# Optimization experiments

Hardware: AMD Instinct MI355X
Metric: run time of the kernel (lower is better)

## Reference

```python
import jax, jax.numpy as jnp
import numpy as np

HIDDEN = 1024
HEADS = 16
HEAD_DIM = HIDDEN // HEADS
LN_EPS = 1e-12


def _layer_norm(x, gamma, beta, eps=LN_EPS):
    mu = jnp.mean(x, axis=-1, keepdims=True)
    var = jnp.var(x, axis=-1, keepdims=True)
    return (x - mu) * jax.lax.rsqrt(var + eps) * gamma + beta


def setup_inputs() -> dict:
    key = jax.random.key(0)
    ks = jax.random.split(key, 8)
    B, S = 4, 2048
    hidden_states = jax.random.normal(ks[0], (B, S, HIDDEN), dtype=jnp.float32)
    attention_mask = jnp.zeros((B, 1, 1, S), dtype=jnp.float32)
    scale = 1.0 / np.sqrt(HIDDEN)
    return {
        "hidden_states": hidden_states,
        "attention_mask": attention_mask,
        "ln_gamma": jnp.ones((HIDDEN,), jnp.float32),
        "ln_beta": jnp.zeros((HIDDEN,), jnp.float32),
        "W_qkv": jax.random.normal(ks[1], (HIDDEN, 3 * HIDDEN), jnp.float32) * scale,
        "b_qkv": jnp.zeros((3 * HIDDEN,), jnp.float32),
        "W_out": jax.random.normal(ks[2], (HIDDEN, HIDDEN), jnp.float32) * scale,
        "b_out": jnp.zeros((HIDDEN,), jnp.float32),
    }


def reference(hidden_states, attention_mask, ln_gamma, ln_beta, W_qkv, b_qkv, W_out, b_out):
    B, S, H = hidden_states.shape
    x = _layer_norm(hidden_states, ln_gamma, ln_beta)
    qkv = x @ W_qkv + b_qkv  # [B, S, 3H]
    q, k, v = jnp.split(qkv, 3, axis=-1)
    q = q.reshape(B, S, HEADS, HEAD_DIM)
    k = k.reshape(B, S, HEADS, HEAD_DIM)
    v = v.reshape(B, S, HEADS, HEAD_DIM)
    # scores: [B, heads, q_len, kv_len]
    scores = jnp.einsum("bqhd,bkhd->bhqk", q, k) * (1.0 / np.sqrt(HEAD_DIM))
    scores = scores + attention_mask
    probs = jax.nn.softmax(scores, axis=-1)
    attn = jnp.einsum("bhqk,bkhd->bqhd", probs, v).reshape(B, S, H)
    out = attn @ W_out + b_out
    out = out + hidden_states  # residual (dropout is identity at p=0)
    return out
```

## Files before the change

kernel.cpp:

```cpp
#include <hip/hip_runtime.h>

#define SEQ 2048
#define HID 1024
#define NHEAD 16
#define HDIM 64
#define NB 4
#define NTOK (NB * SEQ)
#define NQKV (3 * HID)
#define LOG2E 1.44269504088896f
#define QSCALE (0.125f * LOG2E)

typedef __attribute__((ext_vector_type(8))) short bf16x8;
typedef __attribute__((ext_vector_type(4))) float f32x4;


__device__ __forceinline__ void glds16(const void* g, void* l) {
  __builtin_amdgcn_global_load_lds(
      (const __attribute__((address_space(1))) void*)g,
      (__attribute__((address_space(3))) void*)l, 16, 0, 0);
}

__device__ __forceinline__ ushort f2bf(float f) {
  union { float f; unsigned int u; } a; a.f = f;
  unsigned int u = a.u;
  return (ushort)((u + 0x7fffu + ((u >> 16) & 1u)) >> 16);
}

__device__ __forceinline__ unsigned int pack2bf_rh(float a, float b) {
  return __builtin_amdgcn_perm(__float_as_uint(b) + 0x8000u,
                               __float_as_uint(a) + 0x8000u, 0x07060302u);
}


__global__ __launch_bounds__(256) void ln_kernel(const float* __restrict__ x,
                                                 const float* __restrict__ g,
                                                 const float* __restrict__ be,
                                                 ushort* __restrict__ y) {
  const int row = blockIdx.x;
  const int tid = threadIdx.x;
  const float4 v = ((const float4*)(x + (size_t)row * HID))[tid];
  float s  = v.x + v.y + v.z + v.w;
  float sq = v.x * v.x + v.y * v.y + v.z * v.z + v.w * v.w;
  for (int o = 1; o < 64; o <<= 1) { s += __shfl_xor(s, o, 64); sq += __shfl_xor(sq, o, 64); }
  __shared__ float as_[4], aq_[4];
  const int wv = tid >> 6;
  if ((tid & 63) == 0) { as_[wv] = s; aq_[wv] = sq; }
  __syncthreads();
  s  = as_[0] + as_[1] + as_[2] + as_[3];
  sq = aq_[0] + aq_[1] + aq_[2] + aq_[3];
  const float mu  = s * (1.0f / HID);
  const float var = sq * (1.0f / HID) - mu * mu;
  const float rs  = rsqrtf(var + 1e-12f);
  const float4 gv = ((const float4*)g)[tid];
  const float4 bv = ((const float4*)be)[tid];
  ushort4 o;
  o.x = f2bf((v.x - mu) * rs * gv.x + bv.x);
  o.y = f2bf((v.y - mu) * rs * gv.y + bv.y);
  o.z = f2bf((v.z - mu) * rs * gv.z + bv.z);
  o.w = f2bf((v.w - mu) * rs * gv.w + bv.w);
  ((ushort4*)(y + (size_t)row * HID))[tid] = o;
}


__global__ __launch_bounds__(256) void transpose_cvt2(const float* __restrict__ W0,
                                                      ushort* __restrict__ T0,
                                                      const float* __restrict__ W1,
                                                      ushort* __restrict__ T1) {
  const float* W; ushort* WT; int C;
  if (blockIdx.z == 0) { W = W0; WT = T0; C = NQKV; }
  else { if (blockIdx.x >= HID / 32) return; W = W1; WT = T1; C = HID; }
  const int R = HID;
  __shared__ float t[32][33];
  const int c0 = blockIdx.x * 32, r0 = blockIdx.y * 32;
  const int tx = threadIdx.x & 31, ty = threadIdx.x >> 5;
  for (int j = 0; j < 4; ++j)
    t[ty + j * 8][tx] = W[(size_t)(r0 + ty + j * 8) * C + c0 + tx];
  __syncthreads();
  for (int j = 0; j < 4; ++j)
    WT[(size_t)(c0 + ty + j * 8) * R + r0 + tx] = f2bf(t[tx][ty + j * 8]);
}


__global__ __launch_bounds__(256) void v_transpose(const ushort* __restrict__ qkv,
                                                   ushort* __restrict__ vt) {
  __shared__ ushort t[64][66];
  const int s0 = blockIdx.x * 64, h = blockIdx.y, b = blockIdx.z;
  const size_t tokbase = (size_t)b * SEQ;
  for (int e = 0; e < 2; ++e) {
    const int c = e * 256 + threadIdx.x;
    const int sr = c >> 3, dc = c & 7;
    *(uint4*)&t[sr][dc * 8] =
        *(const uint4*)(qkv + (tokbase + s0 + sr) * NQKV + 2 * HID + h * HDIM + dc * 8);
  }
  __syncthreads();
  for (int e = 0; e < 2; ++e) {
    const int c = e * 256 + threadIdx.x;
    const int dr = c >> 3, sc = c & 7;
    ushort tmp[8];
    for (int j = 0; j < 8; ++j) tmp[j] = t[sc * 8 + j][dr];
    *(uint4*)(vt + ((size_t)(b * NHEAD + h) * HDIM + dr) * SEQ + s0 + sc * 8) = *(uint4*)tmp;
  }
}


template <int MODE>
__global__ __launch_bounds__(256) void gemm_bt(const ushort* __restrict__ A,
                                               const ushort* __restrict__ Bt,
                                               const float* __restrict__ bias,
                                               const float* __restrict__ resid,
                                               ushort* __restrict__ obf,
                                               float* __restrict__ of32,
                                               int M, int N, int K) {
  __shared__ ushort As[128 * 64];
  __shared__ ushort Bs[128 * 64];
  const int tid = threadIdx.x;
  const int lane = tid & 63, wv = tid >> 6;
  const int q = lane >> 4, li = lane & 15;
  const int m0 = blockIdx.y * 128, n0 = blockIdx.x * 128;
  const int wm = (wv >> 1) * 64, wn = (wv & 1) * 64;
  f32x4 acc[4][4] = {};

  for (int kb = 0; kb < K; kb += 64) {
    for (int e = 0; e < 4; ++e) {
      const int chunk = (wv * 4 + e) * 64 + lane;
      const int row = chunk >> 3, slot = chunk & 7;
      const int kc = slot ^ (row & 7);
      glds16(A  + (size_t)(m0 + row) * K + kb + kc * 8, As + (wv * 4 + e) * 512);
      glds16(Bt + (size_t)(n0 + row) * K + kb + kc * 8, Bs + (wv * 4 + e) * 512);
    }
    __syncthreads();
    for (int ks = 0; ks < 2; ++ks) {
      const int kc = ks * 4 + q;
      bf16x8 af[4], bfr[4];
      for (int mi = 0; mi < 4; ++mi) {
        const int row = wm + mi * 16 + li;
        af[mi] = *(const bf16x8*)(As + (row * 8 + (kc ^ (row & 7))) * 8);
      }
      for (int ni = 0; ni < 4; ++ni) {
        const int row = wn + ni * 16 + li;
        bfr[ni] = *(const bf16x8*)(Bs + (row * 8 + (kc ^ (row & 7))) * 8);
      }
      for (int mi = 0; mi < 4; ++mi)
        for (int ni = 0; ni < 4; ++ni)
          acc[mi][ni] = __builtin_amdgcn_mfma_f32_16x16x32_bf16(af[mi], bfr[ni], acc[mi][ni], 0, 0, 0);
    }
    __syncthreads();
  }

  const float qs = (MODE == 0 && n0 < HID) ? QSCALE : 1.0f;
  for (int ni = 0; ni < 4; ++ni) {
    const int col = n0 + wn + ni * 16 + li;
    const float bvs = bias[col] * qs;
    for (int mi = 0; mi < 4; ++mi) {
      for (int r = 0; r < 4; ++r) {
        const int row = m0 + wm + mi * 16 + q * 4 + r;
        const float v = fmaf(acc[mi][ni][r], qs, bvs);
        if (MODE == 0) obf[(size_t)row * N + col] = f2bf(v);
        else           of32[(size_t)row * N + col] = v + resid[(size_t)row * N + col];
      }
    }
  }
}


__global__ __launch_bounds__(256) void flash_attn(const ushort* __restrict__ qkv,
                                                  const ushort* __restrict__ vt,
                                                  const float* __restrict__ mask,
                                                  ushort* __restrict__ outa) {
  __shared__ ushort KV[2][8192];
  const int tid = threadIdx.x, lane = tid & 63, wv = tid >> 6;
  const int quad = lane >> 4, li = lane & 15;
  const int wq = wv * 32;

  const int L = blockIdx.x + 16 * blockIdx.y + 256 * blockIdx.z;
  const int xcd = L & 7, rrem = L >> 3;
  const int p = (rrem >> 4) * 8 + xcd;
  const int qt = rrem & 15, h = p & 15, b = p >> 4;

  const size_t tokbase = (size_t)b * SEQ;
  const size_t vtbase = (size_t)(b * NHEAD + h) * HDIM * SEQ;
  const float* mrow = mask + (size_t)b * SEQ;

  for (int e = 0; e < 4; ++e) {
    const int c = (wv * 4 + e) * 64 + lane;
    const int row = c >> 3, slot = c & 7;
    const int kc = slot ^ (row & 7);
    glds16(qkv + (tokbase + qt * 128 + row) * NQKV + h * HDIM + kc * 8,
           &KV[0][0] + (wv * 4 + e) * 512);
  }
  __syncthreads();

  bf16x8 qf[2][2];
  for (int ks = 0; ks < 2; ++ks) {
    const int kc = ks * 4 + quad;
    for (int nq = 0; nq < 2; ++nq) {
      const int row = wq + nq * 16 + li;
      qf[ks][nq] = *(const bf16x8*)(&KV[0][0] + (row * 8 + (kc ^ (row & 7))) * 8);
    }
  }
  __syncthreads();

  int koff[2][4], voff[2][4];
  for (int ks = 0; ks < 2; ++ks) {
    const int kc = ks * 4 + quad;
    for (int i = 0; i < 4; ++i) {
      const int row = i * 16 + li;
      koff[ks][i] = (row * 8 + (kc ^ (row & 7))) * 8;
      voff[ks][i] = koff[ks][i] + 4096;
    }
  }
  const ushort* ksrc[2];
  const ushort* vsrc[2];
  for (int e = 0; e < 2; ++e) {
    const int c = (wv * 2 + e) * 64 + lane;
    const int row = c >> 3, slot = c & 7;
    const int kc = slot ^ (row & 7);
    const int gkv = (row & 0x23) | ((row & 0x0c) << 1) | ((row & 0x10) >> 2);
    ksrc[e] = qkv + (tokbase + gkv) * NQKV + HID + h * HDIM + kc * 8;
    vsrc[e] = vt + vtbase + (size_t)row * SEQ + kc * 8;
  }

  const unsigned int one2 = 0x3F803F80u;
  bf16x8 ones;
  for (int j = 0; j < 4; ++j) ((unsigned int*)&ones)[j] = one2;

  f32x4 accO[2][4] = {};
  f32x4 accL[2] = {};

  auto stage_kv = [&](int t, int buf) {
    const int kv0 = t * 64;
    for (int e = 0; e < 2; ++e) {
      glds16(ksrc[e] + (size_t)kv0 * NQKV, &KV[buf][0] + (wv * 2 + e) * 512);
      glds16(vsrc[e] + kv0,                &KV[buf][4096] + (wv * 2 + e) * 512);
    }
  };

  auto compute = [&](int t, int buf) {
    const int kv0 = t * 64;
    const ushort* Kb = &KV[buf][0];

    float4 mk[4];
    for (int mkv = 0; mkv < 4; ++mkv)
      mk[mkv] = *(const float4*)(mrow + kv0 + (mkv >> 1) * 32 + quad * 8 + (mkv & 1) * 4);

    f32x4 sc[2][4] = {};
    for (int ks = 0; ks < 2; ++ks) {
      bf16x8 kf[4];
      for (int mkv = 0; mkv < 4; ++mkv)
        kf[mkv] = *(const bf16x8*)(Kb + koff[ks][mkv]);
      for (int nq = 0; nq < 2; ++nq)
        for (int mkv = 0; mkv < 4; ++mkv)
          sc[nq][mkv] = __builtin_amdgcn_mfma_f32_16x16x32_bf16(kf[mkv], qf[ks][nq], sc[nq][mkv], 0, 0, 0);
    }

    unsigned int pk[2][4][2];
    for (int nq = 0; nq < 2; ++nq) {
      for (int mkv = 0; mkv < 4; ++mkv) {
        const float p0 = __builtin_amdgcn_exp2f(fmaf(mk[mkv].x, LOG2E, sc[nq][mkv][0]));
        const float p1 = __builtin_amdgcn_exp2f(fmaf(mk[mkv].y, LOG2E, sc[nq][mkv][1]));
        const float p2 = __builtin_amdgcn_exp2f(fmaf(mk[mkv].z, LOG2E, sc[nq][mkv][2]));
        const float p3 = __builtin_amdgcn_exp2f(fmaf(mk[mkv].w, LOG2E, sc[nq][mkv][3]));
        pk[nq][mkv][0] = pack2bf_rh(p0, p1);
        pk[nq][mkv][1] = pack2bf_rh(p2, p3);
      }
    }

    for (int ks = 0; ks < 2; ++ks) {
      bf16x8 vf[4];
      for (int nd = 0; nd < 4; ++nd)
        vf[nd] = *(const bf16x8*)(Kb + voff[ks][nd]);
      for (int mq = 0; mq < 2; ++mq) {
        bf16x8 pf;
        ((unsigned int*)&pf)[0] = pk[mq][2 * ks][0];
        ((unsigned int*)&pf)[1] = pk[mq][2 * ks][1];
        ((unsigned int*)&pf)[2] = pk[mq][2 * ks + 1][0];
        ((unsigned int*)&pf)[3] = pk[mq][2 * ks + 1][1];
        for (int nd = 0; nd < 4; ++nd)
          accO[mq][nd] = __builtin_amdgcn_mfma_f32_16x16x32_bf16(pf, vf[nd], accO[mq][nd], 0, 0, 0);
        accL[mq] = __builtin_amdgcn_mfma_f32_16x16x32_bf16(pf, ones, accL[mq], 0, 0, 0);
      }
    }
  };

  stage_kv(0, 0);
  for (int t = 0; t < SEQ / 64; t += 2) {
    __syncthreads();
    stage_kv(t + 1, 1);
    compute(t, 0);
    __syncthreads();
    if (t + 2 < SEQ / 64) stage_kv(t + 2, 0);
    compute(t + 1, 1);
  }

  for (int mq = 0; mq < 2; ++mq)
    for (int r = 0; r < 4; ++r) {
      const float inv = 1.0f / accL[mq][r];
      const size_t tok = tokbase + qt * 128 + wq + mq * 16 + quad * 4 + r;
      for (int nd = 0; nd < 4; ++nd)
        outa[tok * HID + h * HDIM + nd * 16 + li] = f2bf(accO[mq][nd][r] * inv);
    }
}


extern "C" void kernel_launch(void* const* d_in, const int* in_sizes, int n_in,
                              void* d_out, int out_size, void* d_ws, size_t ws_size,
                              hipStream_t stream) {
  const float* hidden = (const float*)d_in[0];
  const float* mask   = (const float*)d_in[1];
  const float* gamma  = (const float*)d_in[2];
  const float* beta   = (const float*)d_in[3];
  const float* Wqkv   = (const float*)d_in[4];
  const float* bqkv   = (const float*)d_in[5];
  const float* Wout   = (const float*)d_in[6];
  const float* bout   = (const float*)d_in[7];
  float* out = (float*)d_out;

  char* ws = (char*)d_ws;
  ushort* x_bf  = (ushort*)(ws);
  ushort* vtb   = (ushort*)(ws);
  ushort* wqkvT = (ushort*)(ws + ((size_t)16 << 20));
  ushort* woutT = (ushort*)(ws + ((size_t)22 << 20));
  ushort* qkvb  = (ushort*)(ws + ((size_t)24 << 20));
  ushort* attnb = (ushort*)(ws + ((size_t)72 << 20));

  ln_kernel<<<NTOK, 256, 0, stream>>>(hidden, gamma, beta, x_bf);
  transpose_cvt2<<<dim3(NQKV / 32, HID / 32, 2), 256, 0, stream>>>(Wqkv, wqkvT, Wout, woutT);
  gemm_bt<0><<<dim3(NQKV / 128, NTOK / 128), 256, 0, stream>>>(
      x_bf, wqkvT, bqkv, nullptr, qkvb, nullptr, NTOK, NQKV, HID);
  v_transpose<<<dim3(SEQ / 64, NHEAD, NB), 256, 0, stream>>>(qkvb, vtb);
  flash_attn<<<dim3(SEQ / 128, NHEAD, NB), 256, 0, stream>>>(qkvb, vtb, mask, attnb);
  gemm_bt<1><<<dim3(HID / 128, NTOK / 128), 256, 0, stream>>>(
      attnb, woutT, bout, hidden, nullptr, out, NTOK, HID, HID);
}
```

Baseline: 310.6 us.

## Software-pipeline QK^T of next tile with softmax-PV of current tile in flash attention

Splits the K/V shared buffers into a double-buffered K and a triple-buffered V ring. Each iteration computes the QK^T scores for tile t+1 while doing exp and PV for tile t, so MFMA work can overlap with exp and conversion work. It also prefetches two tiles ahead and swaps the manual round-half bf16 pack for the hardware v_cvt_pk_bf16_f32 instruction. The cost is more registers for two score buffers and more LDS, which may lower occupancy.

```diff
diff --git a/kernel.cpp b/kernel.cpp
--- a/kernel.cpp
+++ b/kernel.cpp
@@ -26,9 +26,10 @@
   return (ushort)((u + 0x7fffu + ((u >> 16) & 1u)) >> 16);
 }
 
-__device__ __forceinline__ unsigned int pack2bf_rh(float a, float b) {
-  return __builtin_amdgcn_perm(__float_as_uint(b) + 0x8000u,
-                               __float_as_uint(a) + 0x8000u, 0x07060302u);
+__device__ __forceinline__ unsigned int cvtpk(float a, float b) {
+  unsigned int r;
+  asm("v_cvt_pk_bf16_f32 %0, %1, %2" : "=v"(r) : "v"(a), "v"(b));
+  return r;
 }
 
 
@@ -167,10 +168,12 @@
                                                   const ushort* __restrict__ vt,
                                                   const float* __restrict__ mask,
                                                   ushort* __restrict__ outa) {
-  __shared__ ushort KV[2][8192];
+  __shared__ ushort Kbuf[2][4096];
+  __shared__ ushort Vbuf[3][4096];
   const int tid = threadIdx.x, lane = tid & 63, wv = tid >> 6;
   const int quad = lane >> 4, li = lane & 15;
   const int wq = wv * 32;
+  constexpr int NT = SEQ / 64;
 
   const int L = blockIdx.x + 16 * blockIdx.y + 256 * blockIdx.z;
   const int xcd = L & 7, rrem = L >> 3;
@@ -180,14 +183,36 @@
   const size_t tokbase = (size_t)b * SEQ;
   const size_t vtbase = (size_t)(b * NHEAD + h) * HDIM * SEQ;
   const float* mrow = mask + (size_t)b * SEQ;
+
+  unsigned ksoff[2], vsoff[2];
+  for (int e = 0; e < 2; ++e) {
+    const int c = (wv * 2 + e) * 64 + lane;
+    const int row = c >> 3, slot = c & 7;
+    const int kc = slot ^ (row & 7);
+    const int gkv = (row & 0x23) | ((row & 0x0c) << 1) | ((row & 0x10) >> 2);
+    ksoff[e] = (unsigned)((tokbase + gkv) * NQKV + HID + h * HDIM + kc * 8);
+    vsoff[e] = (unsigned)(vtbase + (size_t)row * SEQ + kc * 8);
+  }
+
+  auto stage_k = [&](int t, int buf) {
+    const unsigned kadd = (unsigned)(t * 64 * NQKV);
+    for (int e = 0; e < 2; ++e)
+      glds16(qkv + ksoff[e] + kadd, &Kbuf[buf][0] + (wv * 2 + e) * 512);
+  };
+  auto stage_v = [&](int t, unsigned vs) {
+    const unsigned vadd = (unsigned)(t * 64);
+    for (int e = 0; e < 2; ++e)
+      glds16(vt + vsoff[e] + vadd, &Vbuf[0][0] + vs + (wv * 2 + e) * 512);
+  };
 
   for (int e = 0; e < 4; ++e) {
     const int c = (wv * 4 + e) * 64 + lane;
     const int row = c >> 3, slot = c & 7;
     const int kc = slot ^ (row & 7);
     glds16(qkv + (tokbase + qt * 128 + row) * NQKV + h * HDIM + kc * 8,
-           &KV[0][0] + (wv * 4 + e) * 512);
-  }
+           &Kbuf[0][0] + (wv * 4 + e) * 512);
+  }
+  stage_v(0, 0);
   __syncthreads();
 
   bf16x8 qf[2][2];
@@ -195,101 +220,102 @@
     const int kc = ks * 4 + quad;
     for (int nq = 0; nq < 2; ++nq) {
       const int row = wq + nq * 16 + li;
-      qf[ks][nq] = *(const bf16x8*)(&KV[0][0] + (row * 8 + (kc ^ (row & 7))) * 8);
-    }
-  }
-  __syncthreads();
-
-  int koff[2][4], voff[2][4];
+      qf[ks][nq] = *(const bf16x8*)(&Kbuf[0][0] + (row * 8 + (kc ^ (row & 7))) * 8);
+    }
+  }
+  __syncthreads();
+
+  int koff[2][4];
   for (int ks = 0; ks < 2; ++ks) {
     const int kc = ks * 4 + quad;
     for (int i = 0; i < 4; ++i) {
       const int row = i * 16 + li;
       koff[ks][i] = (row * 8 + (kc ^ (row & 7))) * 8;
-      voff[ks][i] = koff[ks][i] + 4096;
-    }
-  }
-  const ushort* ksrc[2];
-  const ushort* vsrc[2];
-  for (int e = 0; e < 2; ++e) {
-    const int c = (wv * 2 + e) * 64 + lane;
-    const int row = c >> 3, slot = c & 7;
-    const int kc = slot ^ (row & 7);
-    const int gkv = (row & 0x23) | ((row & 0x0c) << 1) | ((row & 0x10) >> 2);
-    ksrc[e] = qkv + (tokbase + gkv) * NQKV + HID + h * HDIM + kc * 8;
-    vsrc[e] = vt + vtbase + (size_t)row * SEQ + kc * 8;
-  }
+    }
+  }
+
+  stage_k(0, 0); stage_k(1, 1); stage_v(1, 4096);
+  __syncthreads();
 
   const unsigned int one2 = 0x3F803F80u;
   bf16x8 ones;
   for (int j = 0; j < 4; ++j) ((unsigned int*)&ones)[j] = one2;
+  const f32x4 zero4 = {0.f, 0.f, 0.f, 0.f};
 
   f32x4 accO[2][4] = {};
   f32x4 accL[2] = {};
-
-  auto stage_kv = [&](int t, int buf) {
-    const int kv0 = t * 64;
-    for (int e = 0; e < 2; ++e) {
-      glds16(ksrc[e] + (size_t)kv0 * NQKV, &KV[buf][0] + (wv * 2 + e) * 512);
-      glds16(vsrc[e] + kv0,                &KV[buf][4096] + (wv * 2 + e) * 512);
-    }
-  };
-
-  auto compute = [&](int t, int buf) {
-    const int kv0 = t * 64;
-    const ushort* Kb = &KV[buf][0];
-
-    float4 mk[4];
-    for (int mkv = 0; mkv < 4; ++mkv)
-      mk[mkv] = *(const float4*)(mrow + kv0 + (mkv >> 1) * 32 + quad * 8 + (mkv & 1) * 4);
-
-    f32x4 sc[2][4] = {};
+  f32x4 scA[2][4], scB[2][4];
+
+  {
+    const ushort* Kb = &Kbuf[0][0];
     for (int ks = 0; ks < 2; ++ks) {
       bf16x8 kf[4];
-      for (int mkv = 0; mkv < 4; ++mkv)
-        kf[mkv] = *(const bf16x8*)(Kb + koff[ks][mkv]);
+      for (int m = 0; m < 4; ++m) kf[m] = *(const bf16x8*)(Kb + koff[ks][m]);
       for (int nq = 0; nq < 2; ++nq)
-        for (int mkv = 0; mkv < 4; ++mkv)
-          sc[nq][mkv] = __builtin_amdgcn_mfma_f32_16x16x32_bf16(kf[mkv], qf[ks][nq], sc[nq][mkv], 0, 0, 0);
-    }
-
-    unsigned int pk[2][4][2];
-    for (int nq = 0; nq < 2; ++nq) {
-      for (int mkv = 0; mkv < 4; ++mkv) {
-        const float p0 = __builtin_amdgcn_exp2f(fmaf(mk[mkv].x, LOG2E, sc[nq][mkv][0]));
-        const float p1 = __builtin_amdgcn_exp2f(fmaf(mk[mkv].y, LOG2E, sc[nq][mkv][1]));
-        const float p2 = __builtin_amdgcn_exp2f(fmaf(mk[mkv].z, LOG2E, sc[nq][mkv][2]));
-        const float p3 = __builtin_amdgcn_exp2f(fmaf(mk[mkv].w, LOG2E, sc[nq][mkv][3]));
-        pk[nq][mkv][0] = pack2bf_rh(p0, p1);
-        pk[nq][mkv][1] = pack2bf_rh(p2, p3);
-      }
-    }
-
+        for (int m = 0; m < 4; ++m)
+          scA[nq][m] = __builtin_amdgcn_mfma_f32_16x16x32_bf16(
+              kf[m], qf[ks][nq], ks == 0 ? zero4 : scA[nq][m], 0, 0, 0);
+    }
+  }
+
+  unsigned sV0 = 0, sV1 = 4096, sV2 = 8192;
+
+  auto iter = [&](int t, f32x4 (&scC)[2][4], f32x4 (&scN)[2][4]) {
+    __syncthreads();
+    const int kv0 = t * 64;
+    float4 mk01[2];
+    for (int m = 0; m < 2; ++m)
+      mk01[m] = *(const float4*)(mrow + kv0 + quad * 8 + m * 4);
+    if (t + 2 < NT) { stage_k(t + 2, t & 1); stage_v(t + 2, sV2); }
+    if (t + 1 < NT) {
+      const ushort* Kb = &Kbuf[(t + 1) & 1][0];
+      for (int ks = 0; ks < 2; ++ks) {
+        bf16x8 kf[4];
+        for (int m = 0; m < 4; ++m) kf[m] = *(const bf16x8*)(Kb + koff[ks][m]);
+        for (int nq = 0; nq < 2; ++nq)
+          for (int m = 0; m < 4; ++m)
+            scN[nq][m] = __builtin_amdgcn_mfma_f32_16x16x32_bf16(
+                kf[m], qf[ks][nq], ks == 0 ? zero4 : scN[nq][m], 0, 0, 0);
+      }
+    }
+    float4 mk23[2];
+    for (int m = 0; m < 2; ++m)
+      mk23[m] = *(const float4*)(mrow + kv0 + 32 + quad * 8 + m * 4);
+
+    const ushort* Vb = &Vbuf[0][0] + sV0;
     for (int ks = 0; ks < 2; ++ks) {
       bf16x8 vf[4];
       for (int nd = 0; nd < 4; ++nd)
-        vf[nd] = *(const bf16x8*)(Kb + voff[ks][nd]);
+        vf[nd] = *(const bf16x8*)(Vb + koff[ks][nd]);
+      unsigned int pk[2][2][2];
+      for (int nq = 0; nq < 2; ++nq)
+        for (int mm = 0; mm < 2; ++mm) {
+          const int m = 2 * ks + mm;
+          const float4 mkv = ks == 0 ? mk01[mm] : mk23[mm];
+          const float p0 = __builtin_amdgcn_exp2f(fmaf(mkv.x, LOG2E, scC[nq][m][0]));
+          const float p1 = __builtin_amdgcn_exp2f(fmaf(mkv.y, LOG2E, scC[nq][m][1]));
+          const float p2 = __builtin_amdgcn_exp2f(fmaf(mkv.z, LOG2E, scC[nq][m][2]));
+          const float p3 = __builtin_amdgcn_exp2f(fmaf(mkv.w, LOG2E, scC[nq][m][3]));
+          pk[nq][mm][0] = cvtpk(p0, p1);
+          pk[nq][mm][1] = cvtpk(p2, p3);
+        }
       for (int mq = 0; mq < 2; ++mq) {
         bf16x8 pf;
-        ((unsigned int*)&pf)[0] = pk[mq][2 * ks][0];
-        ((unsigned int*)&pf)[1] = pk[mq][2 * ks][1];
-        ((unsigned int*)&pf)[2] = pk[mq][2 * ks + 1][0];
-        ((unsigned int*)&pf)[3] = pk[mq][2 * ks + 1][1];
+        ((unsigned int*)&pf)[0] = pk[mq][0][0];
+        ((unsigned int*)&pf)[1] = pk[mq][0][1];
+        ((unsigned int*)&pf)[2] = pk[mq][1][0];
+        ((unsigned int*)&pf)[3] = pk[mq][1][1];
         for (int nd = 0; nd < 4; ++nd)
           accO[mq][nd] = __builtin_amdgcn_mfma_f32_16x16x32_bf16(pf, vf[nd], accO[mq][nd], 0, 0, 0);
         accL[mq] = __builtin_amdgcn_mfma_f32_16x16x32_bf16(pf, ones, accL[mq], 0, 0, 0);
       }
     }
+    const unsigned tmp = sV0; sV0 = sV1; sV1 = sV2; sV2 = tmp;
   };
 
-  stage_kv(0, 0);
-  for (int t = 0; t < SEQ / 64; t += 2) {
-    __syncthreads();
-    stage_kv(t + 1, 1);
-    compute(t, 0);
-    __syncthreads();
-    if (t + 2 < SEQ / 64) stage_kv(t + 2, 0);
-    compute(t + 1, 1);
+  for (int t = 0; t < NT; t += 2) {
+    iter(t,     scA, scB);
+    iter(t + 1, scB, scA);
   }
 
   for (int mq = 0; mq < 2; ++mq)
```

Measured after the change: 312.5 us. Within noise of the previous version (+0.6%).
